# Kernel tuning notes

Measured on AMD Instinct MI355X. Metric: run time of the kernel, lower is better.

## Reference

```python
import jax, jax.numpy as jnp
import numpy as np

EMBED_DIM = 1024
NUM_HEADS = 16
HEAD_DIM = EMBED_DIM // NUM_HEADS
SCALE = HEAD_DIM ** -0.5


def setup_inputs() -> dict:
    key = jax.random.key(0)
    k_x, k_wqkv, k_bqkv, k_wo, k_bo = jax.random.split(key, 5)
    B, T, C = 2, 2048, EMBED_DIM
    bound = 1.0 / np.sqrt(C)
    return {
        "x": jax.random.normal(k_x, (B, T, C), dtype=jnp.float32),
        "w_qkv": jax.random.uniform(k_wqkv, (C, 3 * C), jnp.float32, -bound, bound),
        "b_qkv": jax.random.uniform(k_bqkv, (3 * C,), jnp.float32, -bound, bound),
        "w_out": jax.random.uniform(k_wo, (C, C), jnp.float32, -bound, bound),
        "b_out": jax.random.uniform(k_bo, (C,), jnp.float32, -bound, bound),
    }


def reference(x, w_qkv, b_qkv, w_out, b_out):
    B, T, C = x.shape
    H, D = NUM_HEADS, HEAD_DIM
    qkv = x @ w_qkv + b_qkv                      # [B,T,3C]
    q, k, v = jnp.split(qkv, 3, axis=-1)         # each [B,T,C]
    q = q.reshape(B, T, H, D).transpose(0, 2, 1, 3)  # [B,H,T,D]
    k = k.reshape(B, T, H, D).transpose(0, 2, 1, 3)
    v = v.reshape(B, T, H, D).transpose(0, 2, 1, 3)
    scores = jnp.einsum("bhqd,bhkd->bhqk", q, k) * SCALE  # [B,H,T,T]
    weights = jax.nn.softmax(scores, axis=-1)
    out = jnp.einsum("bhqk,bhkd->bhqd", weights, v)       # [B,H,T,D]
    concat = out.transpose(0, 2, 1, 3).reshape(B, T, C)
    return concat @ w_out + b_out
```

## Files before the change

kernel.cpp:

```cpp
#include <hip/hip_runtime.h>

typedef _Float16 f16;
typedef _Float16 f16x8 __attribute__((ext_vector_type(8)));
typedef _Float16 f16x4 __attribute__((ext_vector_type(4)));
typedef float f32x4 __attribute__((ext_vector_type(4)));
typedef float f32x16 __attribute__((ext_vector_type(16)));
typedef unsigned int u32x4 __attribute__((ext_vector_type(4)));

#define SCALE_Q (0.125f * 1.44269504088896f)

__device__ __forceinline__ f32x4 mfma16x16x32(f16x8 a, f16x8 b, f32x4 c) {
  return __builtin_amdgcn_mfma_f32_16x16x32_f16(a, b, c, 0, 0, 0);
}
__device__ __forceinline__ f32x16 mfma32x32x16(f16x8 a, f16x8 b, f32x16 c) {
  return __builtin_amdgcn_mfma_f32_32x32x16_f16(a, b, c, 0, 0, 0);
}

__device__ __forceinline__ float fexp2(float x) {
  return __builtin_amdgcn_exp2f(x);
}

typedef const __attribute__((address_space(1))) void* gptr1;
typedef __attribute__((address_space(3))) void* lptr3;
__device__ __forceinline__ void gload_lds16(const void* g, void* l) {
  __builtin_amdgcn_global_load_lds((gptr1)g, (lptr3)l, 16, 0, 0);
}

__device__ __forceinline__ unsigned pk2(float a, float b) {
  return __builtin_bit_cast(unsigned, __builtin_amdgcn_cvt_pkrtz(a, b));
}

__global__ __launch_bounds__(256)
void prep(const float* __restrict__ x, f16* __restrict__ xh,
          const float* __restrict__ w_qkv, f16* __restrict__ wqkvT,
          const float* __restrict__ w_out, f16* __restrict__ woutT) {
  __shared__ float tile[32][33];
  const int bid = blockIdx.x;
  const int tid = threadIdx.x;
  if (bid < 4096) {
    int i = bid * 256 + tid;
    float4 v = reinterpret_cast<const float4*>(x)[i];
    f16x4 o = {(f16)v.x, (f16)v.y, (f16)v.z, (f16)v.w};
    reinterpret_cast<f16x4*>(xh)[i] = o;
    return;
  }
  const float* in;
  f16* out;
  int bx, by, R, Cin;
  if (bid < 7168) {
    int t = bid - 4096;
    in = w_qkv; out = wqkvT; R = 1024; Cin = 3072;
    bx = (t % 96) * 32; by = (t / 96) * 32;
  } else {
    int t = bid - 7168;
    in = w_out; out = woutT; R = 1024; Cin = 1024;
    bx = (t % 32) * 32; by = (t / 32) * 32;
  }
  int tx = tid & 31, ty = tid >> 5;
#pragma unroll
  for (int i = ty; i < 32; i += 8)
    tile[i][tx] = in[(size_t)(by + i) * Cin + bx + tx];
  __syncthreads();
#pragma unroll
  for (int i = ty; i < 32; i += 8)
    out[(size_t)(bx + i) * R + by + tx] = (f16)tile[tx][i];
}

__global__ __launch_bounds__(256)
void gemm_qkv(const f16* __restrict__ A, const f16* __restrict__ Bt,
              const float* __restrict__ bias, f16* __restrict__ qQ,
              f16* __restrict__ kP, f16* __restrict__ vP) {
  constexpr int BM = 128, BN = 128, BK = 32, K = 1024;
  __shared__ f16 As[BM * BK];
  __shared__ f16 Bs[BN * BK];
  const int tid = threadIdx.x;
  const int l = tid & 63;
  const int w = tid >> 6;
  const int wr = w >> 1, wc = w & 1;
  const int bid = blockIdx.x;
  const int xcd = bid & 7, idx = bid >> 3;
  const int xg = xcd & 3, yg = xcd >> 2;
  const int mx = xg * 8 + (idx & 7);
  const int ny = yg * 12 + (idx >> 3);
  const int bm = mx * BM, bn = ny * BN;
  const int l15 = l & 15, lhi = l >> 4;

  f32x4 acc[4][4] = {};

  const char* Ab = (const char*)A;
  const char* Bb = (const char*)Bt;
  const size_t rowbytes = (size_t)K * 2;

  for (int kt = 0; kt < K; kt += BK) {
    __syncthreads();
#pragma unroll
    for (int c = 0; c < 2; ++c) {
      int o = tid * 16 + c * 4096;
      int r = o >> 6;
      int cb = o & 63;
      gload_lds16(Ab + (size_t)(bm + r) * rowbytes + (size_t)kt * 2 + cb, (char*)As + o);
      gload_lds16(Bb + (size_t)(bn + r) * rowbytes + (size_t)kt * 2 + cb, (char*)Bs + o);
    }
    __syncthreads();

    f16x8 af[4], bf[4];
#pragma unroll
    for (int i = 0; i < 4; ++i)
      af[i] = *reinterpret_cast<const f16x8*>(&As[(wr * 64 + i * 16 + l15) * BK + 8 * lhi]);
#pragma unroll
    for (int i = 0; i < 4; ++i)
      bf[i] = *reinterpret_cast<const f16x8*>(&Bs[(wc * 64 + i * 16 + l15) * BK + 8 * lhi]);
#pragma unroll
    for (int i = 0; i < 4; ++i)
#pragma unroll
      for (int j = 0; j < 4; ++j)
        acc[i][j] = mfma16x16x32(af[i], bf[j], acc[i][j]);
  }

  const int region = bn >> 10;
#pragma unroll
  for (int i = 0; i < 4; ++i) {
#pragma unroll
    for (int j = 0; j < 4; ++j) {
      int gr0 = bm + wr * 64 + i * 16 + 4 * lhi;
      int gc = bn + wc * 64 + j * 16 + l15;
      float bia = bias[gc];
      if (region == 0) {
#pragma unroll
        for (int r = 0; r < 4; ++r) {
          float v = (acc[i][j][r] + bia) * SCALE_Q;
          qQ[(size_t)(gr0 + r) * 1024 + gc] = (f16)v;
        }
      } else if (region == 1) {
        int dloc = gc - 1024;
        int h = dloc >> 6, dd = dloc & 63;
        int kd = dd >> 4, hi8 = (dd >> 3) & 1, j8 = dd & 7;
        int bb = gr0 >> 11;
        int pair = bb * 16 + h;
#pragma unroll
        for (int r = 0; r < 4; ++r) {
          int key = (gr0 + r) & 2047;
          int t32 = key >> 5, l31k = key & 31;
          size_t idxp = ((((size_t)pair * 64 + t32) * 4 + kd) * 64 + (hi8 * 32 + l31k)) * 8 + j8;
          kP[idxp] = (f16)(acc[i][j][r] + bia);
        }
      } else {
        int dloc = gc - 2048;
        int h = dloc >> 6, dd = dloc & 63;
        int dhalf = dd >> 5, l31v = dd & 31;
        int bb = gr0 >> 11;
        int pair = bb * 16 + h;
        int key = gr0 & 2047;
        int t64 = key >> 6;
        int k6 = key & 63;
        int ks = k6 >> 4, hiv = (k6 >> 3) & 1, jv = k6 & 7;
        int rr = dhalf * 4 + ks;
        size_t idxp = ((((size_t)pair * 32 + t64) * 8 + rr) * 64 + (hiv * 32 + l31v)) * 8 + jv;
        f16x4 ov;
#pragma unroll
        for (int r = 0; r < 4; ++r) ov[r] = (f16)(acc[i][j][r] + bia);
        *reinterpret_cast<f16x4*>(&vP[idxp]) = ov;
      }
    }
  }
}

__global__ __launch_bounds__(256)
void gemm_out(const f16* __restrict__ A, const f16* __restrict__ Bt,
              const float* __restrict__ bias, float* __restrict__ outf) {
  constexpr int BM = 128, BN = 64, BK = 32, K = 1024, N = 1024;
  __shared__ f16 As[BM * BK];
  __shared__ f16 Bs[BN * BK];
  const int tid = threadIdx.x;
  const int l = tid & 63;
  const int w = tid >> 6;
  const int bid = blockIdx.x;
  const int xcd = bid & 7, idx = bid >> 3;
  const int mx = xcd * 4 + (idx & 3);
  const int ny = idx >> 2;
  const int bm = mx * BM, bn = ny * BN;
  const int l15 = l & 15, lhi = l >> 4;

  f32x4 acc[2][4] = {};

  const char* Ab = (const char*)A;
  const char* Bb = (const char*)Bt;
  const size_t rowbytes = (size_t)K * 2;

  for (int kt = 0; kt < K; kt += BK) {
    __syncthreads();
#pragma unroll
    for (int c = 0; c < 2; ++c) {
      int o = tid * 16 + c * 4096;
      int r = o >> 6;
      int cb = o & 63;
      gload_lds16(Ab + (size_t)(bm + r) * rowbytes + (size_t)kt * 2 + cb, (char*)As + o);
    }
    {
      int o = tid * 16;
      int r = o >> 6;
      int cb = o & 63;
      gload_lds16(Bb + (size_t)(bn + r) * rowbytes + (size_t)kt * 2 + cb, (char*)Bs + o);
    }
    __syncthreads();

    f16x8 af[2], bf[4];
#pragma unroll
    for (int i = 0; i < 2; ++i)
      af[i] = *reinterpret_cast<const f16x8*>(&As[(w * 32 + i * 16 + l15) * BK + 8 * lhi]);
#pragma unroll
    for (int j = 0; j < 4; ++j)
      bf[j] = *reinterpret_cast<const f16x8*>(&Bs[(j * 16 + l15) * BK + 8 * lhi]);
#pragma unroll
    for (int i = 0; i < 2; ++i)
#pragma unroll
      for (int j = 0; j < 4; ++j)
        acc[i][j] = mfma16x16x32(af[i], bf[j], acc[i][j]);
  }

#pragma unroll
  for (int i = 0; i < 2; ++i) {
#pragma unroll
    for (int j = 0; j < 4; ++j) {
      int gr0 = bm + w * 32 + i * 16 + 4 * lhi;
      int gc = bn + j * 16 + l15;
      float b = bias[gc];
#pragma unroll
      for (int r = 0; r < 4; ++r)
        outf[(size_t)(gr0 + r) * N + gc] = acc[i][j][r] + b;
    }
  }
}

__global__ __launch_bounds__(256, 2)
void attn_kernel(const f16* __restrict__ qQ, const f16* __restrict__ kP,
                 const f16* __restrict__ vP, f16* __restrict__ outh) {
  constexpr int T = 2048;
  __shared__ float mo[4096];
  __shared__ float MlBuf[2][64];

  const int tid = threadIdx.x;
  const int l = tid & 63;
  const int w = tid >> 6;
  const int wq = w >> 1;
  const int grp = w & 1;
  const int l31 = l & 31, hi = l >> 5;

  const int bid = blockIdx.x;
  const int pair = bid & 31;
  const int b = pair >> 4;
  const int h = pair & 15;
  const int qt = bid >> 5;

  const int q0 = qt * 64 + wq * 32;

  f16x8 bq[4];
  {
    const f16* qp = qQ + (size_t)(b * T + q0 + l31) * 1024 + h * 64 + hi * 8;
#pragma unroll
    for (int kd = 0; kd < 4; ++kd)
      bq[kd] = *reinterpret_cast<const f16x8*>(qp + kd * 16);
  }

  const f16* Kp = kP + (size_t)pair * 131072;
  const f16* Vp = vP + (size_t)pair * 131072;

  f32x16 o0 = {}, o1 = {};
  float l_r = 0.f;
  const int tbase = grp * 16;

#define LOADK_TO(AK, T64)                                                      \
  do {                                                                         \
    _Pragma("unroll") for (int kt = 0; kt < 2; ++kt)                           \
    _Pragma("unroll") for (int kd = 0; kd < 4; ++kd)                           \
      AK[kt][kd] = *reinterpret_cast<const f16x8*>(                            \
          Kp + ((((size_t)(T64) * 2 + kt) * 4 + kd) * 64 + l) * 8);            \
  } while (0)

#define TILE_BODY(AKC, AKN, TT, TN)                                            \
  do {                                                                         \
    const int t64g = tbase + (TT);                                             \
                         \
    f16x8 av0[4], av1[4];                                                      \
    _Pragma("unroll") for (int ks = 0; ks < 4; ++ks) {                         \
      av0[ks] = *reinterpret_cast<const f16x8*>(                               \
          Vp + (((size_t)t64g * 8 + ks) * 64 + l) * 8);                        \
      av1[ks] = *reinterpret_cast<const f16x8*>(                               \
          Vp + (((size_t)t64g * 8 + 4 + ks) * 64 + l) * 8);                    \
    }                                                                          \
    f32x16 s0 = {}, s1 = {};                                                   \
    __builtin_amdgcn_s_setprio(1);                                             \
    _Pragma("unroll") for (int kd = 0; kd < 4; ++kd)                           \
      s0 = mfma32x32x16(AKC[0][kd], bq[kd], s0);                               \
    _Pragma("unroll") for (int kd = 0; kd < 4; ++kd)                           \
      s1 = mfma32x32x16(AKC[1][kd], bq[kd], s1);                               \
    __builtin_amdgcn_s_setprio(0);                                             \
      \
    LOADK_TO(AKN, tbase + (TN));                                               \
    float sm[16];                                                              \
    _Pragma("unroll") for (int r = 0; r < 16; ++r) {                           \
      s0[r] = fexp2(s0[r]);                                                    \
      s1[r] = fexp2(s1[r]);                                                    \
      sm[r] = s0[r] + s1[r];                                                   \
    }                                                                          \
    _Pragma("unroll") for (int st = 8; st > 0; st >>= 1)                       \
      _Pragma("unroll") for (int r = 0; r < st; ++r) sm[r] += sm[r + st];      \
    l_r += sm[0] + __shfl_xor(sm[0], 32);                                      \
    f16x8 bp[4];                                                               \
    _Pragma("unroll") for (int kt = 0; kt < 2; ++kt) {                         \
      _Pragma("unroll") for (int s2 = 0; s2 < 2; ++s2) {                       \
        u32x4 wd;                                                              \
        _Pragma("unroll") for (int u = 0; u < 2; ++u) {                        \
          float a0 = kt ? s1[8 * s2 + 2 * u] : s0[8 * s2 + 2 * u];             \
          float a1 = kt ? s1[8 * s2 + 2 * u + 1] : s0[8 * s2 + 2 * u + 1];     \
          float b0 = kt ? s1[8 * s2 + 4 + 2 * u] : s0[8 * s2 + 4 + 2 * u];     \
          float b1 = kt ? s1[8 * s2 + 4 + 2 * u + 1] : s0[8 * s2 + 4 + 2 * u + 1]; \
          unsigned wB = pk2(a0, a1);                                           \
          unsigned wA = pk2(b0, b1);                                           \
          unsigned oB = __shfl_xor(wB, 32);                                    \
          unsigned oA = __shfl_xor(wA, 32);                                    \
          wd[u]     = hi ? oA : wB;                                            \
          wd[2 + u] = hi ? wA : oB;                                            \
        }                                                                      \
        bp[2 * kt + s2] = __builtin_bit_cast(f16x8, wd);                       \
      }                                                                        \
    }                                                                          \
    __builtin_amdgcn_s_setprio(1);                                             \
    _Pragma("unroll") for (int ks = 0; ks < 4; ++ks) {                         \
      o0 = mfma32x32x16(av0[ks], bp[ks], o0);                                  \
      o1 = mfma32x32x16(av1[ks], bp[ks], o1);                                  \
    }                                                                          \
    __builtin_amdgcn_s_setprio(0);                                             \
  } while (0)

  f16x8 akA[2][4], akB[2][4];
  LOADK_TO(akA, tbase);
#pragma unroll 1
  for (int t = 0; t < 16; t += 2) {
    TILE_BODY(akA, akB, t, t + 1);
    TILE_BODY(akB, akA, t + 1, (t + 2 < 16 ? t + 2 : 15));
  }

  const int mbase = wq * 2048 + l * 32;
  if (grp == 1) {
#pragma unroll
    for (int k = 0; k < 8; ++k) {
      int ks = k ^ (l & 7);
      f32x4 v;
      if (k < 4) { v = f32x4{o0[4*k], o0[4*k+1], o0[4*k+2], o0[4*k+3]}; }
      else       { int r = 4*(k-4); v = f32x4{o1[r], o1[r+1], o1[r+2], o1[r+3]}; }
      *reinterpret_cast<f32x4*>(&mo[mbase + ks * 4]) = v;
    }
    MlBuf[wq][l] = l_r;
  }
  __syncthreads();
  if (grp == 0) {
    float inv = 1.0f / (l_r + MlBuf[wq][l]);
    f16* orow = outh + (size_t)(b * T + q0 + l31) * 1024 + h * 64;
#pragma unroll
    for (int k = 0; k < 8; ++k) {
      int ks = k ^ (l & 7);
      f32x4 ob = *reinterpret_cast<const f32x4*>(&mo[mbase + ks * 4]);
#pragma unroll
      for (int j = 0; j < 4; ++j) {
        int r = 4 * (k & 3) + j;
        int d = (r & 3) + 8 * (r >> 2) + 4 * hi;
        float own = (k < 4) ? o0[r] : o1[r];
        float val = (own + ob[j]) * inv;
        orow[(k < 4 ? d : d + 32)] = (f16)val;
      }
    }
  }
#undef LOADK_TO
#undef TILE_BODY
}

extern "C" void kernel_launch(void* const* d_in, const int* in_sizes, int n_in,
                              void* d_out, int out_size, void* d_ws, size_t ws_size,
                              hipStream_t stream) {
  const float* x      = (const float*)d_in[0];
  const float* w_qkv  = (const float*)d_in[1];
  const float* b_qkv  = (const float*)d_in[2];
  const float* w_out  = (const float*)d_in[3];
  const float* b_out  = (const float*)d_in[4];
  float* out = (float*)d_out;

  char* ws = (char*)d_ws;
  f16* xh    = (f16*)(ws);
  f16* wqkvT = (f16*)(ws + 8388608);
  f16* woutT = (f16*)(ws + 14680064);
  f16* qQ    = (f16*)(ws + 16777216);
  f16* kP    = (f16*)(ws + 25165824);
  f16* vP    = (f16*)(ws + 33554432);
  f16* attnh = (f16*)(ws + 41943040);

  prep<<<8192, 256, 0, stream>>>(x, xh, w_qkv, wqkvT, w_out, woutT);
  gemm_qkv<<<768, 256, 0, stream>>>(xh, wqkvT, b_qkv, qQ, kP, vP);
  attn_kernel<<<1024, 256, 0, stream>>>(qQ, kP, vP, attnh);
  gemm_out<<<512, 256, 0, stream>>>(attnh, woutT, b_out, out);
}
```

Before: 119.9 us.

## Software-pipeline QK^T one tile ahead of softmax and PV in attention

Restructures the attention loop so that the QK^T MFMAs for the next key tile are issued before the exp/pack/PV work of the current tile. This lets matrix and vector work interleave, and K loads are prefetched two tiles ahead. The V loads are split, with the second half issued after the P packing. The launch_bounds occupancy hint is dropped to make room for the extra score registers, which may lower occupancy or cause spills.

```diff
diff --git a/kernel.cpp b/kernel.cpp
--- a/kernel.cpp
+++ b/kernel.cpp
@@ -232,9 +232,8 @@
   }
 }
 
-__global__ __launch_bounds__(256, 2)
-void attn_kernel(const f16* __restrict__ qQ, const f16* __restrict__ kP,
-                 const f16* __restrict__ vP, f16* __restrict__ outh) {
+__global__ void attn_kernel(const f16* __restrict__ qQ, const f16* __restrict__ kP,
+                            const f16* __restrict__ vP, f16* __restrict__ outh) {
   constexpr int T = 2048;
   __shared__ float mo[4096];
   __shared__ float MlBuf[2][64];
@@ -268,6 +267,7 @@
   f32x16 o0 = {}, o1 = {};
   float l_r = 0.f;
   const int tbase = grp * 16;
+  const f32x16 vzero = {};
 
 #define LOADK_TO(AK, T64)                                                      \
   do {                                                                         \
@@ -277,31 +277,31 @@
           Kp + ((((size_t)(T64) * 2 + kt) * 4 + kd) * 64 + l) * 8);            \
   } while (0)
 
-#define TILE_BODY(AKC, AKN, TT, TN)                                            \
+#define QK_INTO(S0, S1, AK)                                                    \
+  do {                                                                         \
+    S0 = vzero; S1 = vzero;                                                    \
+    __builtin_amdgcn_s_setprio(1);                                             \
+    _Pragma("unroll") for (int kd = 0; kd < 4; ++kd)                           \
+      S0 = mfma32x32x16(AK[0][kd], bq[kd], S0);                                \
+    _Pragma("unroll") for (int kd = 0; kd < 4; ++kd)                           \
+      S1 = mfma32x32x16(AK[1][kd], bq[kd], S1);                                \
+    __builtin_amdgcn_s_setprio(0);                                             \
+  } while (0)
+
+#define BODY(SC0, SC1, SN0, SN1, AKQ, AKL, TT, TLOAD)                          \
   do {                                                                         \
     const int t64g = tbase + (TT);                                             \
-                         \
-    f16x8 av0[4], av1[4];                                                      \
-    _Pragma("unroll") for (int ks = 0; ks < 4; ++ks) {                         \
+    QK_INTO(SN0, SN1, AKQ);                                                    \
+    LOADK_TO(AKL, tbase + (TLOAD));                                            \
+    f16x8 av0[4];                                                              \
+    _Pragma("unroll") for (int ks = 0; ks < 4; ++ks)                           \
       av0[ks] = *reinterpret_cast<const f16x8*>(                               \
           Vp + (((size_t)t64g * 8 + ks) * 64 + l) * 8);                        \
-      av1[ks] = *reinterpret_cast<const f16x8*>(                               \
-          Vp + (((size_t)t64g * 8 + 4 + ks) * 64 + l) * 8);                    \
-    }                                                                          \
-    f32x16 s0 = {}, s1 = {};                                                   \
-    __builtin_amdgcn_s_setprio(1);                                             \
-    _Pragma("unroll") for (int kd = 0; kd < 4; ++kd)                           \
-      s0 = mfma32x32x16(AKC[0][kd], bq[kd], s0);                               \
-    _Pragma("unroll") for (int kd = 0; kd < 4; ++kd)                           \
-      s1 = mfma32x32x16(AKC[1][kd], bq[kd], s1);                               \
-    __builtin_amdgcn_s_setprio(0);                                             \
-      \
-    LOADK_TO(AKN, tbase + (TN));                                               \
     float sm[16];                                                              \
     _Pragma("unroll") for (int r = 0; r < 16; ++r) {                           \
-      s0[r] = fexp2(s0[r]);                                                    \
-      s1[r] = fexp2(s1[r]);                                                    \
-      sm[r] = s0[r] + s1[r];                                                   \
+      SC0[r] = fexp2(SC0[r]);                                                  \
+      SC1[r] = fexp2(SC1[r]);                                                  \
+      sm[r] = SC0[r] + SC1[r];                                                 \
     }                                                                          \
     _Pragma("unroll") for (int st = 8; st > 0; st >>= 1)                       \
       _Pragma("unroll") for (int r = 0; r < st; ++r) sm[r] += sm[r + st];      \
@@ -311,10 +311,10 @@
       _Pragma("unroll") for (int s2 = 0; s2 < 2; ++s2) {                       \
         u32x4 wd;                                                              \
         _Pragma("unroll") for (int u = 0; u < 2; ++u) {                        \
-          float a0 = kt ? s1[8 * s2 + 2 * u] : s0[8 * s2 + 2 * u];             \
-          float a1 = kt ? s1[8 * s2 + 2 * u + 1] : s0[8 * s2 + 2 * u + 1];     \
-          float b0 = kt ? s1[8 * s2 + 4 + 2 * u] : s0[8 * s2 + 4 + 2 * u];     \
-          float b1 = kt ? s1[8 * s2 + 4 + 2 * u + 1] : s0[8 * s2 + 4 + 2 * u + 1]; \
+          float a0 = kt ? SC1[8 * s2 + 2 * u] : SC0[8 * s2 + 2 * u];           \
+          float a1 = kt ? SC1[8 * s2 + 2 * u + 1] : SC0[8 * s2 + 2 * u + 1];   \
+          float b0 = kt ? SC1[8 * s2 + 4 + 2 * u] : SC0[8 * s2 + 4 + 2 * u];   \
+          float b1 = kt ? SC1[8 * s2 + 4 + 2 * u + 1] : SC0[8 * s2 + 4 + 2 * u + 1]; \
           unsigned wB = pk2(a0, a1);                                           \
           unsigned wA = pk2(b0, b1);                                           \
           unsigned oB = __shfl_xor(wB, 32);                                    \
@@ -325,6 +325,10 @@
         bp[2 * kt + s2] = __builtin_bit_cast(f16x8, wd);                       \
       }                                                                        \
     }                                                                          \
+    f16x8 av1[4];                                                              \
+    _Pragma("unroll") for (int ks = 0; ks < 4; ++ks)                           \
+      av1[ks] = *reinterpret_cast<const f16x8*>(                               \
+          Vp + (((size_t)t64g * 8 + 4 + ks) * 64 + l) * 8);                    \
     __builtin_amdgcn_s_setprio(1);                                             \
     _Pragma("unroll") for (int ks = 0; ks < 4; ++ks) {                         \
       o0 = mfma32x32x16(av0[ks], bp[ks], o0);                                  \
@@ -334,11 +338,14 @@
   } while (0)
 
   f16x8 akA[2][4], akB[2][4];
+  f32x16 sA0, sA1, sB0, sB1;
   LOADK_TO(akA, tbase);
+  QK_INTO(sA0, sA1, akA);
+  LOADK_TO(akB, tbase + 1);
 #pragma unroll 1
   for (int t = 0; t < 16; t += 2) {
-    TILE_BODY(akA, akB, t, t + 1);
-    TILE_BODY(akB, akA, t + 1, (t + 2 < 16 ? t + 2 : 15));
+    BODY(sA0, sA1, sB0, sB1, akB, akA, t, (t + 2 < 16 ? t + 2 : 15));
+    BODY(sB0, sB1, sA0, sA1, akA, akB, t + 1, (t + 3 < 16 ? t + 3 : 15));
   }
 
   const int mbase = wq * 2048 + l * 32;
@@ -372,7 +379,8 @@
     }
   }
 #undef LOADK_TO
-#undef TILE_BODY
+#undef QK_INTO
+#undef BODY
 }
 
 extern "C" void kernel_launch(void* const* d_in, const int* in_sizes, int n_in,
```

New measurement: 308.6 us. 157% more time.
